# Optimization experiments

Measured on AMD Instinct MI355X. Metric: run time of the kernel, lower is better.

Reference implementation:

```python
import jax, jax.numpy as jnp
import numpy as np

D_MODEL = 256
SCALE = jnp.sqrt(jnp.float32(D_MODEL))


def setup_inputs() -> dict:
    key = jax.random.key(0)
    kq, kk, kv = jax.random.split(key, 3)
    B, S, D = 4, 4096, D_MODEL
    Q = jax.random.normal(kq, (B, S, D), dtype=jnp.float32)
    K = jax.random.normal(kk, (B, S, D), dtype=jnp.float32)
    V = jax.random.normal(kv, (B, S, D), dtype=jnp.float32)
    return {"Q": Q, "K": K, "V": V}


def reference(Q, K, V):
    # scores: (B, S, S) = Q @ K^T / sqrt(d_model)
    scores = jnp.einsum('bqd,bkd->bqk', Q, K) / SCALE
    attn = jax.nn.softmax(scores, axis=-1)
    # output: (B, S, D)
    return jnp.einsum('bqk,bkd->bqd', attn, V)
```

## Files before the change

### kernel.cpp

```cpp
#include <hip/hip_runtime.h>
#include <hip/hip_bf16.h>
#include <stdint.h>

#define S_LEN 4096
#define D_DIM 256
#define NBATCH 4
#define NSUP 32

typedef unsigned short u16;
typedef float  f32x4  __attribute__((ext_vector_type(4)));
typedef __bf16 bf16x8 __attribute__((ext_vector_type(8)));
typedef __bf16 bf16x4 __attribute__((ext_vector_type(4)));
typedef short  s16x8  __attribute__((ext_vector_type(8)));
typedef short  s16x4  __attribute__((ext_vector_type(4)));

#define AS1 __attribute__((address_space(1)))
#define AS3 __attribute__((address_space(3)))

__device__ __forceinline__ f32x4 mfma16(bf16x8 a, bf16x8 b, f32x4 c) {
  return __builtin_amdgcn_mfma_f32_16x16x32_bf16(a, b, c, 0, 0, 0);
}

__device__ __forceinline__ s16x4 cvt4(float x, float y, float z, float w) {
  bf16x4 b;
  b[0] = (__bf16)x; b[1] = (__bf16)y; b[2] = (__bf16)z; b[3] = (__bf16)w;
  return __builtin_bit_cast(s16x4, b);
}

__device__ __forceinline__ void gload16(const void* g, void* l) {
  __builtin_amdgcn_global_load_lds((const AS1 unsigned int*)g,
                                   (AS3 unsigned int*)l, 16, 0, 0);
}


__global__ void build_imgs(const float* __restrict__ K, const float* __restrict__ V,
                           u16* __restrict__ kimg, u16* __restrict__ vimg) {
  __shared__ u16 lds[64 * 264];
  const int wg  = blockIdx.x;
  const int tid = threadIdx.x;

  const float* ksrc = K + (size_t)wg * 64 * D_DIM;
  u16*         kdst = kimg + (size_t)wg * 16384;
  #pragma unroll
  for (int i = 0; i < 8; ++i) {
    const int idx = i * 256 + tid;
    const int k = idx >> 5, p = idx & 31;
    const int q = p ^ (k & 7);
    const float* s = ksrc + k * 256 + q * 8;
    float4 f0 = *reinterpret_cast<const float4*>(s);
    float4 f1 = *reinterpret_cast<const float4*>(s + 4);
    s16x8 v = __builtin_shufflevector(cvt4(f0.x, f0.y, f0.z, f0.w),
                                      cvt4(f1.x, f1.y, f1.z, f1.w),
                                      0, 1, 2, 3, 4, 5, 6, 7);
    *reinterpret_cast<s16x8*>(kdst + k * 256 + p * 8) = v;
  }

  const float* vsrc = V + (size_t)wg * 64 * D_DIM;
  u16*         vdst = vimg + (size_t)wg * 16384;
  #pragma unroll
  for (int i = 0; i < 8; ++i) {
    const int idx = i * 256 + tid;
    const int k = idx >> 5, q = idx & 31;
    const float* s = vsrc + k * 256 + q * 8;
    float4 f0 = *reinterpret_cast<const float4*>(s);
    float4 f1 = *reinterpret_cast<const float4*>(s + 4);
    s16x8 v = __builtin_shufflevector(cvt4(f0.x, f0.y, f0.z, f0.w),
                                      cvt4(f1.x, f1.y, f1.z, f1.w),
                                      0, 1, 2, 3, 4, 5, 6, 7);
    *reinterpret_cast<s16x8*>(&lds[k * 264 + q * 8]) = v;
  }
  __syncthreads();
  #pragma unroll
  for (int i = 0; i < 8; ++i) {
    const int idx = i * 256 + tid;
    const int d = idx >> 3, c = idx & 7;
    const int cp = c ^ (d & 7);
    s16x8 o;
    #pragma unroll
    for (int j = 0; j < 8; ++j) {
      const int col = 8 * cp + j;
      const int k = (col & 3) + 4 * (col >> 4) + 16 * ((col >> 2) & 3);
      o[j] = (short)lds[k * 264 + d];
    }
    *reinterpret_cast<s16x8*>(vdst + d * 64 + c * 8) = o;
  }
}

__device__ __forceinline__
void compute_tile(const char* KsB, const char* vpA, const char* vpB,
                  const bf16x8 (&qf)[8], f32x4 (&acc)[16],
                  float& m_run, float& l_run, int g, int h)
{
  const f32x4 fz = {0.f, 0.f, 0.f, 0.f};

  f32x4 st[4];
  __builtin_amdgcn_s_setprio(1);
  #pragma unroll
  for (int t = 0; t < 4; ++t) {
    f32x4 a = fz;
    const int row = t * 16 + h;
    const int sw  = (row & 7) << 4;
    #pragma unroll
    for (int dc = 0; dc < 8; ++dc) {
      s16x8 kfrag = *reinterpret_cast<const s16x8*>(KsB + row * 512 + ((dc * 64 + g * 16) ^ sw));
      a = mfma16(__builtin_bit_cast(bf16x8, kfrag), qf[dc], a);
    }
    st[t] = a;
  }
  __builtin_amdgcn_s_setprio(0);

  float sv[16];
  #pragma unroll
  for (int t = 0; t < 4; ++t) {
    sv[t * 4 + 0] = st[t][0]; sv[t * 4 + 1] = st[t][1];
    sv[t * 4 + 2] = st[t][2]; sv[t * 4 + 3] = st[t][3];
  }
  float tmax = sv[0];
  #pragma unroll
  for (int i = 1; i < 16; ++i) tmax = fmaxf(tmax, sv[i]);
  tmax = fmaxf(tmax, __shfl_xor(tmax, 16));
  tmax = fmaxf(tmax, __shfl_xor(tmax, 32));

  if (!__all(tmax <= m_run + 8.0f)) {
    const float mnew  = fmaxf(m_run, tmax);
    const float alpha = __expf(m_run - mnew);
    l_run *= alpha;
    const float af0 = __shfl(alpha, g * 4 + 0);
    const float af1 = __shfl(alpha, g * 4 + 1);
    const float af2 = __shfl(alpha, g * 4 + 2);
    const float af3 = __shfl(alpha, g * 4 + 3);
    #pragma unroll
    for (int dt = 0; dt < 16; ++dt) {
      acc[dt][0] *= af0; acc[dt][1] *= af1; acc[dt][2] *= af2; acc[dt][3] *= af3;
    }
    m_run = mnew;
  }

  float psum = 0.f;
  #pragma unroll
  for (int i = 0; i < 16; ++i) { sv[i] = __expf(sv[i] - m_run); psum += sv[i]; }
  psum += __shfl_xor(psum, 16);
  psum += __shfl_xor(psum, 32);
  l_run += psum;

  bf16x8 pa0, pa1;
  #pragma unroll
  for (int j = 0; j < 8; ++j) { pa0[j] = (__bf16)sv[j]; pa1[j] = (__bf16)sv[8 + j]; }

  __builtin_amdgcn_s_setprio(1);
  #pragma unroll
  for (int dt = 0; dt < 16; ++dt) {
    s16x8 v0 = *reinterpret_cast<const s16x8*>(vpA + dt * 2048);
    s16x8 v1 = *reinterpret_cast<const s16x8*>(vpB + dt * 2048);
    acc[dt] = mfma16(pa0, __builtin_bit_cast(bf16x8, v0), acc[dt]);
    acc[dt] = mfma16(pa1, __builtin_bit_cast(bf16x8, v1), acc[dt]);
  }
  __builtin_amdgcn_s_setprio(0);
}

__device__ __forceinline__
void stage_img(const u16* KimgB, const u16* VimgB, int T,
               char* KsB, char* VtB, int w, int lane)
{
  const char* ks = (const char*)(KimgB + (size_t)T * 16384) + lane * 16;
  const char* vs = (const char*)(VimgB + (size_t)T * 16384) + lane * 16;
  #pragma unroll
  for (int i = 0; i < 8; ++i) {
    const int off = (i * 4 + w) * 1024;
    gload16(ks + off, KsB + off);
    gload16(vs + off, VtB + off);
  }
}

template<bool USE_WS>
__global__ __launch_bounds__(512, 1)
void attn_fwd_kernel(const float* __restrict__ Qg, const void* __restrict__ Kp,
                     const void* __restrict__ Vp, float* __restrict__ Og)
{
  __shared__ __align__(16) char smem[131072];

  const int wg   = blockIdx.x;
  const int swz  = (wg & 7) * 32 + (wg >> 3);
  const int b    = swz >> 6;
  const int qt   = swz & 63;
  const int tid  = threadIdx.x;
  const int wave = tid >> 6;
  const int lane = tid & 63;
  const int g    = lane >> 4;
  const int h    = lane & 15;
  const int gid  = tid >> 8;
  const int ltid = tid & 255;
  const int wq   = wave & 3;
  const int w    = wave & 3;

  const int kb  = ltid & 15;
  const int dcq = ltid >> 4;
  const int Xw  = 32 * (kb & 3) + 8 * (kb >> 2);

  char* KsB = smem + gid * 65536;
  char* VtB = KsB + 32768;

  const int qbase = qt * 64 + wq * 16;

  bf16x8 qf[8];
  {
    const float* qrow = Qg + ((size_t)b * S_LEN + qbase + h) * D_DIM;
    #pragma unroll
    for (int dc = 0; dc < 8; ++dc) {
      float4 f0 = *reinterpret_cast<const float4*>(qrow + dc * 32 + g * 8);
      float4 f1 = *reinterpret_cast<const float4*>(qrow + dc * 32 + g * 8 + 4);
      bf16x8 q;
      q[0] = (__bf16)(f0.x * 0.0625f); q[1] = (__bf16)(f0.y * 0.0625f);
      q[2] = (__bf16)(f0.z * 0.0625f); q[3] = (__bf16)(f0.w * 0.0625f);
      q[4] = (__bf16)(f1.x * 0.0625f); q[5] = (__bf16)(f1.y * 0.0625f);
      q[6] = (__bf16)(f1.z * 0.0625f); q[7] = (__bf16)(f1.w * 0.0625f);
      qf[dc] = q;
    }
  }

  f32x4 acc[16];
  const f32x4 fz = {0.f, 0.f, 0.f, 0.f};
  #pragma unroll
  for (int i = 0; i < 16; ++i) acc[i] = fz;
  float m_run = -1e30f;
  float l_run = 0.f;

  const char* vpA = VtB + h * 128 + ((32 * g)      ^ ((h & 7) << 4));
  const char* vpB = VtB + h * 128 + ((32 * g + 16) ^ ((h & 7) << 4));

  if constexpr (USE_WS) {
    const u16* KimgB = (const u16*)Kp + (size_t)b * 64 * 16384;
    const u16* VimgB = (const u16*)Vp + (size_t)b * 64 * 16384;

    if (gid == 0) stage_img(KimgB, VimgB, 0, KsB, VtB, w, lane);
    __syncthreads();

    for (int s = 0; s < NSUP; ++s) {
      if (gid == 0) compute_tile(KsB, vpA, vpB, qf, acc, m_run, l_run, g, h);
      else          stage_img(KimgB, VimgB, 2 * s + 1, KsB, VtB, w, lane);
      __syncthreads();
      if (gid == 0) { if (s < NSUP - 1) stage_img(KimgB, VimgB, 2 * s + 2, KsB, VtB, w, lane); }
      else          compute_tile(KsB, vpA, vpB, qf, acc, m_run, l_run, g, h);
      __syncthreads();
    }

  } else {
    const float* Kf = (const float*)Kp + (size_t)b * S_LEN * D_DIM;
    const float* Vf = (const float*)Vp + (size_t)b * S_LEN * D_DIM;
    for (int s = 0; s < NSUP; ++s) {
      const int kt = 2 * s + gid;
      __syncthreads();
      #pragma unroll
      for (int i = 0; i < 16; ++i) {
        int flat = i * 256 + ltid;
        int kk = flat >> 6;
        int d  = (flat & 63) * 4;
        float4 fk = *reinterpret_cast<const float4*>(Kf + (size_t)(kt * 64 + kk) * D_DIM + d);
        *reinterpret_cast<s16x4*>(KsB + kk * 512 + ((d * 2) ^ ((kk & 7) << 4))) = cvt4(fk.x, fk.y, fk.z, fk.w);
      }
      {
        s16x8 lo[4], hi[4];
        #pragma unroll
        for (int r = 0; r < 4; ++r) {
          const float* src = Vf + (size_t)(kt * 64 + kb * 4 + r) * D_DIM + dcq * 16;
          float4 f0 = *reinterpret_cast<const float4*>(src);
          float4 f1 = *reinterpret_cast<const float4*>(src + 4);
          float4 f2 = *reinterpret_cast<const float4*>(src + 8);
          float4 f3 = *reinterpret_cast<const float4*>(src + 12);
          lo[r] = __builtin_shufflevector(cvt4(f0.x, f0.y, f0.z, f0.w),
                                          cvt4(f1.x, f1.y, f1.z, f1.w), 0, 1, 2, 3, 4, 5, 6, 7);
          hi[r] = __builtin_shufflevector(cvt4(f2.x, f2.y, f2.z, f2.w),
                                          cvt4(f3.x, f3.y, f3.z, f3.w), 0, 1, 2, 3, 4, 5, 6, 7);
        }
        #pragma unroll
        for (int j = 0; j < 8; ++j) {
          s16x4 c0, c1;
          c0[0] = lo[0][j]; c0[1] = lo[1][j]; c0[2] = lo[2][j]; c0[3] = lo[3][j];
          c1[0] = hi[0][j]; c1[1] = hi[1][j]; c1[2] = hi[2][j]; c1[3] = hi[3][j];
          const int d0 = dcq * 16 + j;
          const int d1 = d0 + 8;
          *reinterpret_cast<s16x4*>(VtB + d0 * 128 + (Xw ^ ((d0 & 7) << 4))) = c0;
          *reinterpret_cast<s16x4*>(VtB + d1 * 128 + (Xw ^ ((d1 & 7) << 4))) = c1;
        }
      }
      __syncthreads();
      compute_tile(KsB, vpA, vpB, qf, acc, m_run, l_run, g, h);
    }
  }

  __syncthreads();
  float2* mlM = reinterpret_cast<float2*>(smem + 65536);
  if (gid == 1) {
    const int bw = wave - 4;
    char* base = smem + bw * 16384 + lane * 256;
    #pragma unroll
    for (int dt = 0; dt < 16; ++dt) {
      float4 v; v.x = acc[dt][0]; v.y = acc[dt][1]; v.z = acc[dt][2]; v.w = acc[dt][3];
      *reinterpret_cast<float4*>(base + (dt * 16 ^ ((lane & 7) << 4))) = v;
    }
    if (g == 0) { float2 ml; ml.x = m_run; ml.y = l_run; mlM[bw * 16 + h] = ml; }
  }
  __syncthreads();
  if (gid == 0) {
    const float2 ml = mlM[wave * 16 + h];
    const float mB = ml.x, lB = ml.y;
    const float m  = fmaxf(m_run, mB);
    const float sA = __expf(m_run - m);
    const float sB = __expf(mB - m);
    const float l  = l_run * sA + lB * sB;
    float aA[4], aB[4], inv[4];
    #pragma unroll
    for (int r = 0; r < 4; ++r) {
      aA[r]  = __shfl(sA, g * 4 + r);
      aB[r]  = __shfl(sB, g * 4 + r);
      inv[r] = 1.f / __shfl(l, g * 4 + r);
    }
    const char* base = smem + wave * 16384 + lane * 256;
    float* orow0 = Og + ((size_t)b * S_LEN + qbase) * D_DIM;
    #pragma unroll
    for (int dt = 0; dt < 16; ++dt) {
      float4 ab = *reinterpret_cast<const float4*>(base + (dt * 16 ^ ((lane & 7) << 4)));
      orow0[(size_t)(g * 4 + 0) * D_DIM + h + dt * 16] = (acc[dt][0] * aA[0] + ab.x * aB[0]) * inv[0];
      orow0[(size_t)(g * 4 + 1) * D_DIM + h + dt * 16] = (acc[dt][1] * aA[1] + ab.y * aB[1]) * inv[1];
      orow0[(size_t)(g * 4 + 2) * D_DIM + h + dt * 16] = (acc[dt][2] * aA[2] + ab.z * aB[2]) * inv[2];
      orow0[(size_t)(g * 4 + 3) * D_DIM + h + dt * 16] = (acc[dt][3] * aA[3] + ab.w * aB[3]) * inv[3];
    }
  }
}

extern "C" void kernel_launch(void* const* d_in, const int* in_sizes, int n_in,
                              void* d_out, int out_size, void* d_ws, size_t ws_size,
                              hipStream_t stream)
{
  const float* Q = (const float*)d_in[0];
  const float* K = (const float*)d_in[1];
  const float* V = (const float*)d_in[2];
  float* O = (float*)d_out;

  const size_t nelem = (size_t)NBATCH * S_LEN * D_DIM;
  const size_t need  = 2 * nelem * sizeof(u16);

  if (ws_size >= need) {
    u16* Kimg = (u16*)d_ws;
    u16* Vimg = Kimg + nelem;
    build_imgs<<<256, 256, 0, stream>>>(K, V, Kimg, Vimg);
    attn_fwd_kernel<true><<<256, 512, 0, stream>>>(Q, (const void*)Kimg, (const void*)Vimg, O);
  } else {
    attn_fwd_kernel<false><<<256, 512, 0, stream>>>(Q, (const void*)K, (const void*)V, O);
  }
}
```

Baseline: 124.4 us.

## Split KV sequence in two halves with 32-row tiles and merge kernel

Adds a split-KV path. Each query tile is processed by two workgroups, one per half of the key sequence, using 32-row K/V tiles, smaller LDS and two workgroups per CU. Partial outputs and (m,l) statistics go to workspace and a separate merge kernel combines them. The aim is to double the grid from 256 to 512 workgroups for better CU occupancy, at the cost of extra global traffic for the fp32 partials, a third kernel launch, and half-width MFMA tiles per step.

```diff
diff --git a/kernel.cpp b/kernel.cpp
--- a/kernel.cpp
+++ b/kernel.cpp
@@ -5,7 +5,9 @@
 #define S_LEN 4096
 #define D_DIM 256
 #define NBATCH 4
-#define NSUP 32
+#define KVBLK 32
+#define NSUP32 32
+#define NSUP64 32
 
 typedef unsigned short u16;
 typedef float  f32x4  __attribute__((ext_vector_type(4)));
@@ -33,8 +35,60 @@
 }
 
 
-__global__ void build_imgs(const float* __restrict__ K, const float* __restrict__ V,
-                           u16* __restrict__ kimg, u16* __restrict__ vimg) {
+__global__ void build_imgs32(const float* __restrict__ K, const float* __restrict__ V,
+                             u16* __restrict__ kimg, u16* __restrict__ vimg) {
+  __shared__ u16 lds[KVBLK * 264];
+  const int wg  = blockIdx.x;
+  const int tid = threadIdx.x;
+
+  const float* ksrc = K + (size_t)wg * KVBLK * D_DIM;
+  u16*         kdst = kimg + (size_t)wg * 8192;
+  #pragma unroll
+  for (int i = 0; i < 4; ++i) {
+    const int idx = i * 256 + tid;
+    const int k = idx >> 5, p = idx & 31;
+    const int q = p ^ (k & 7);
+    const float* s = ksrc + k * 256 + q * 8;
+    float4 f0 = *reinterpret_cast<const float4*>(s);
+    float4 f1 = *reinterpret_cast<const float4*>(s + 4);
+    s16x8 v = __builtin_shufflevector(cvt4(f0.x, f0.y, f0.z, f0.w),
+                                      cvt4(f1.x, f1.y, f1.z, f1.w),
+                                      0, 1, 2, 3, 4, 5, 6, 7);
+    *reinterpret_cast<s16x8*>(kdst + k * 256 + p * 8) = v;
+  }
+
+  const float* vsrc = V + (size_t)wg * KVBLK * D_DIM;
+  u16*         vdst = vimg + (size_t)wg * 8192;
+  #pragma unroll
+  for (int i = 0; i < 4; ++i) {
+    const int idx = i * 256 + tid;
+    const int k = idx >> 5, q = idx & 31;
+    const float* s = vsrc + k * 256 + q * 8;
+    float4 f0 = *reinterpret_cast<const float4*>(s);
+    float4 f1 = *reinterpret_cast<const float4*>(s + 4);
+    s16x8 v = __builtin_shufflevector(cvt4(f0.x, f0.y, f0.z, f0.w),
+                                      cvt4(f1.x, f1.y, f1.z, f1.w),
+                                      0, 1, 2, 3, 4, 5, 6, 7);
+    *reinterpret_cast<s16x8*>(&lds[k * 264 + q * 8]) = v;
+  }
+  __syncthreads();
+  const int d = tid;
+  const int s = ((d >> 4) ^ d) & 3;
+  #pragma unroll
+  for (int c = 0; c < 4; ++c) {
+    const int gp = c ^ s;
+    s16x8 o;
+    #pragma unroll
+    for (int ii = 0; ii < 8; ++ii) {
+      const int k = 16 * (ii >> 2) + 4 * gp + (ii & 3);
+      o[ii] = (short)lds[k * 264 + d];
+    }
+    *reinterpret_cast<s16x8*>(vdst + d * 32 + c * 8) = o;
+  }
+}
+
+__global__ void build_imgs64(const float* __restrict__ K, const float* __restrict__ V,
+                             u16* __restrict__ kimg, u16* __restrict__ vimg) {
   __shared__ u16 lds[64 * 264];
   const int wg  = blockIdx.x;
   const int tid = threadIdx.x;
@@ -87,9 +141,79 @@
 }
 
 __device__ __forceinline__
-void compute_tile(const char* KsB, const char* vpA, const char* vpB,
-                  const bf16x8 (&qf)[8], f32x4 (&acc)[16],
-                  float& m_run, float& l_run, int g, int h)
+void compute_tile32(const char* KsB, const char* VtB,
+                    const bf16x8 (&qf)[8], f32x4 (&acc)[16],
+                    float& m_run, float& l_run, int g, int h)
+{
+  const f32x4 fz = {0.f, 0.f, 0.f, 0.f};
+
+  f32x4 st[2];
+  st[0] = fz; st[1] = fz;
+  __builtin_amdgcn_s_setprio(1);
+  #pragma unroll
+  for (int t = 0; t < 2; ++t) {
+    const int row = t * 16 + h;
+    const int sw  = (row & 7) << 4;
+    #pragma unroll
+    for (int dc = 0; dc < 8; ++dc) {
+      s16x8 kf = *reinterpret_cast<const s16x8*>(KsB + row * 512 + ((dc * 64 + g * 16) ^ sw));
+      st[t] = mfma16(__builtin_bit_cast(bf16x8, kf), qf[dc], st[t]);
+    }
+  }
+  __builtin_amdgcn_s_setprio(0);
+
+  float sv[8];
+  #pragma unroll
+  for (int t = 0; t < 2; ++t) {
+    sv[t * 4 + 0] = st[t][0]; sv[t * 4 + 1] = st[t][1];
+    sv[t * 4 + 2] = st[t][2]; sv[t * 4 + 3] = st[t][3];
+  }
+  float tmax = sv[0];
+  #pragma unroll
+  for (int i = 1; i < 8; ++i) tmax = fmaxf(tmax, sv[i]);
+  tmax = fmaxf(tmax, __shfl_xor(tmax, 16));
+  tmax = fmaxf(tmax, __shfl_xor(tmax, 32));
+
+  if (!__all(tmax <= m_run + 8.0f)) {
+    const float mnew  = fmaxf(m_run, tmax);
+    const float alpha = __expf(m_run - mnew);
+    l_run *= alpha;
+    float af[4];
+    #pragma unroll
+    for (int r = 0; r < 4; ++r) af[r] = __shfl(alpha, g * 4 + r);
+    #pragma unroll
+    for (int dt = 0; dt < 16; ++dt) {
+      acc[dt][0] *= af[0]; acc[dt][1] *= af[1];
+      acc[dt][2] *= af[2]; acc[dt][3] *= af[3];
+    }
+    m_run = mnew;
+  }
+
+  float psum = 0.f;
+  #pragma unroll
+  for (int i = 0; i < 8; ++i) { sv[i] = __expf(sv[i] - m_run); psum += sv[i]; }
+  psum += __shfl_xor(psum, 16);
+  psum += __shfl_xor(psum, 32);
+  l_run += psum;
+
+  bf16x8 pa;
+  #pragma unroll
+  for (int j = 0; j < 8; ++j) pa[j] = (__bf16)sv[j];
+
+  __builtin_amdgcn_s_setprio(1);
+  #pragma unroll
+  for (int dt = 0; dt < 16; ++dt) {
+    const int d = dt * 16 + h;
+    s16x8 vf = *reinterpret_cast<const s16x8*>(VtB + d * 64 + ((16 * g) ^ (((dt ^ h) & 3) << 4)));
+    acc[dt] = mfma16(pa, __builtin_bit_cast(bf16x8, vf), acc[dt]);
+  }
+  __builtin_amdgcn_s_setprio(0);
+}
+
+__device__ __forceinline__
+void compute_tile64(const char* KsB, const char* vpA, const char* vpB,
+                    const bf16x8 (&qf)[8], f32x4 (&acc)[16],
+                    float& m_run, float& l_run, int g, int h)
 {
   const f32x4 fz = {0.f, 0.f, 0.f, 0.f};
 
@@ -159,8 +283,21 @@
 }
 
 __device__ __forceinline__
-void stage_img(const u16* KimgB, const u16* VimgB, int T,
-               char* KsB, char* VtB, int w, int lane)
+void stage_img32(const u16* KimgB, const u16* VimgB, int T,
+                 char* KsB, char* VtB, int gl)
+{
+  const char* ks = (const char*)(KimgB + (size_t)T * 8192) + gl * 16;
+  const char* vs = (const char*)(VimgB + (size_t)T * 8192) + gl * 16;
+  #pragma unroll
+  for (int i = 0; i < 4; ++i) {
+    gload16(ks + i * 4096, KsB + gl * 16 + i * 4096);
+    gload16(vs + i * 4096, VtB + gl * 16 + i * 4096);
+  }
+}
+
+__device__ __forceinline__
+void stage_img64(const u16* KimgB, const u16* VimgB, int T,
+                 char* KsB, char* VtB, int w, int lane)
 {
   const char* ks = (const char*)(KimgB + (size_t)T * 16384) + lane * 16;
   const char* vs = (const char*)(VimgB + (size_t)T * 16384) + lane * 16;
@@ -172,9 +309,144 @@
   }
 }
 
+__global__ __launch_bounds__(512, 2)
+void attn_partial_kernel(const float* __restrict__ Qg, const u16* __restrict__ Kimg,
+                         const u16* __restrict__ Vimg, float* __restrict__ Opart,
+                         float2* __restrict__ mlG)
+{
+  __shared__ __align__(16) char smem[66560];
+
+  const int wg   = blockIdx.x;
+  const int swz  = (wg & 7) * 64 + (wg >> 3);
+  const int b    = swz >> 7;
+  const int half = (swz >> 6) & 1;
+  const int qt   = swz & 63;
+  const int tid  = threadIdx.x;
+  const int wave = tid >> 6;
+  const int lane = tid & 63;
+  const int g    = lane >> 4;
+  const int h    = lane & 15;
+  const int gid  = tid >> 8;
+  const int ltid = tid & 255;
+  const int wq   = wave & 3;
+
+  char* KsB = smem + gid * 32768;
+  char* VtB = KsB + 16384;
+  float2* mlM = reinterpret_cast<float2*>(smem + 65536);
+
+  const int qbase = qt * 64 + wq * 16;
+
+  bf16x8 qf[8];
+  {
+    const float* qrow = Qg + ((size_t)b * S_LEN + qbase + h) * D_DIM;
+    #pragma unroll
+    for (int dc = 0; dc < 8; ++dc) {
+      float4 f0 = *reinterpret_cast<const float4*>(qrow + dc * 32 + g * 8);
+      float4 f1 = *reinterpret_cast<const float4*>(qrow + dc * 32 + g * 8 + 4);
+      bf16x8 q;
+      q[0] = (__bf16)(f0.x * 0.0625f); q[1] = (__bf16)(f0.y * 0.0625f);
+      q[2] = (__bf16)(f0.z * 0.0625f); q[3] = (__bf16)(f0.w * 0.0625f);
+      q[4] = (__bf16)(f1.x * 0.0625f); q[5] = (__bf16)(f1.y * 0.0625f);
+      q[6] = (__bf16)(f1.z * 0.0625f); q[7] = (__bf16)(f1.w * 0.0625f);
+      qf[dc] = q;
+    }
+  }
+
+  f32x4 acc[16];
+  const f32x4 fz = {0.f, 0.f, 0.f, 0.f};
+  #pragma unroll
+  for (int i = 0; i < 16; ++i) acc[i] = fz;
+  float m_run = -1e30f;
+  float l_run = 0.f;
+
+  const u16* KimgB = Kimg + (size_t)b * 128 * 8192 + (size_t)half * 64 * 8192;
+  const u16* VimgB = Vimg + (size_t)b * 128 * 8192 + (size_t)half * 64 * 8192;
+
+  if (gid == 0) stage_img32(KimgB, VimgB, 0, KsB, VtB, ltid);
+  __syncthreads();
+  for (int s = 0; s < NSUP32; ++s) {
+    if (gid == 0) compute_tile32(KsB, VtB, qf, acc, m_run, l_run, g, h);
+    else          stage_img32(KimgB, VimgB, 2 * s + 1, KsB, VtB, ltid);
+    __syncthreads();
+    if (gid == 0) { if (s < NSUP32 - 1) stage_img32(KimgB, VimgB, 2 * s + 2, KsB, VtB, ltid); }
+    else          compute_tile32(KsB, VtB, qf, acc, m_run, l_run, g, h);
+    __syncthreads();
+  }
+
+  __syncthreads();
+  if (gid == 1) {
+    const int bw = wave - 4;
+    char* base = smem + bw * 16384 + lane * 256;
+    #pragma unroll
+    for (int dt = 0; dt < 16; ++dt) {
+      float4 v; v.x = acc[dt][0]; v.y = acc[dt][1]; v.z = acc[dt][2]; v.w = acc[dt][3];
+      *reinterpret_cast<float4*>(base + (dt * 16 ^ ((lane & 7) << 4))) = v;
+    }
+    if (g == 0) { float2 ml; ml.x = m_run; ml.y = l_run; mlM[bw * 16 + h] = ml; }
+  }
+  __syncthreads();
+  if (gid == 0) {
+    const float2 ml = mlM[wave * 16 + h];
+    const float mB = ml.x, lB = ml.y;
+    const float m  = fmaxf(m_run, mB);
+    const float sA = __expf(m_run - m);
+    const float sB = __expf(mB - m);
+    const float l  = l_run * sA + lB * sB;
+    float aA[4], aB[4];
+    #pragma unroll
+    for (int r = 0; r < 4; ++r) {
+      aA[r] = __shfl(sA, g * 4 + r);
+      aB[r] = __shfl(sB, g * 4 + r);
+    }
+    const char* base = smem + wave * 16384 + lane * 256;
+    float* orow0 = Opart + (size_t)half * NBATCH * S_LEN * D_DIM
+                 + ((size_t)b * S_LEN + qbase) * D_DIM;
+    #pragma unroll
+    for (int dt = 0; dt < 16; ++dt) {
+      float4 ab = *reinterpret_cast<const float4*>(base + (dt * 16 ^ ((lane & 7) << 4)));
+      orow0[(size_t)(g * 4 + 0) * D_DIM + h + dt * 16] = acc[dt][0] * aA[0] + ab.x * aB[0];
+      orow0[(size_t)(g * 4 + 1) * D_DIM + h + dt * 16] = acc[dt][1] * aA[1] + ab.y * aB[1];
+      orow0[(size_t)(g * 4 + 2) * D_DIM + h + dt * 16] = acc[dt][2] * aA[2] + ab.z * aB[2];
+      orow0[(size_t)(g * 4 + 3) * D_DIM + h + dt * 16] = acc[dt][3] * aA[3] + ab.w * aB[3];
+    }
+    if (g == 0) {
+      float2 o; o.x = m; o.y = l;
+      mlG[(size_t)half * NBATCH * S_LEN + (size_t)b * S_LEN + qbase + h] = o;
+    }
+  }
+}
+
+__global__ void merge_halves(const float* __restrict__ Opart,
+                             const float2* __restrict__ mlG,
+                             float* __restrict__ Og)
+{
+  const size_t TOT = (size_t)NBATCH * S_LEN * D_DIM;
+  const size_t f4base = ((size_t)blockIdx.x * 256 + threadIdx.x) * 4;
+  const size_t row = (f4base * 4) / D_DIM;
+  const float2 ml0 = mlG[row];
+  const float2 ml1 = mlG[(size_t)NBATCH * S_LEN + row];
+  const float m  = fmaxf(ml0.x, ml1.x);
+  const float w0 = __expf(ml0.x - m);
+  const float w1 = __expf(ml1.x - m);
+  const float inv = 1.f / (ml0.y * w0 + ml1.y * w1);
+  const float4* p0 = reinterpret_cast<const float4*>(Opart) + f4base;
+  const float4* p1 = reinterpret_cast<const float4*>(Opart + TOT) + f4base;
+  float4* po = reinterpret_cast<float4*>(Og) + f4base;
+  #pragma unroll
+  for (int i = 0; i < 4; ++i) {
+    float4 a = p0[i], c = p1[i];
+    float4 o;
+    o.x = (a.x * w0 + c.x * w1) * inv;
+    o.y = (a.y * w0 + c.y * w1) * inv;
+    o.z = (a.z * w0 + c.z * w1) * inv;
+    o.w = (a.w * w0 + c.w * w1) * inv;
+    po[i] = o;
+  }
+}
+
 template<bool USE_WS>
 __global__ __launch_bounds__(512, 1)
-void attn_fwd_kernel(const float* __restrict__ Qg, const void* __restrict__ Kp,
+void attn_r21_kernel(const float* __restrict__ Qg, const void* __restrict__ Kp,
                      const void* __restrict__ Vp, float* __restrict__ Og)
 {
   __shared__ __align__(16) char smem[131072];
@@ -232,22 +504,22 @@
     const u16* KimgB = (const u16*)Kp + (size_t)b * 64 * 16384;
     const u16* VimgB = (const u16*)Vp + (size_t)b * 64 * 16384;
 
-    if (gid == 0) stage_img(KimgB, VimgB, 0, KsB, VtB, w, lane);
+    if (gid == 0) stage_img64(KimgB, VimgB, 0, KsB, VtB, w, lane);
     __syncthreads();
 
-    for (int s = 0; s < NSUP; ++s) {
-      if (gid == 0) compute_tile(KsB, vpA, vpB, qf, acc, m_run, l_run, g, h);
-      else          stage_img(KimgB, VimgB, 2 * s + 1, KsB, VtB, w, lane);
+    for (int s = 0; s < NSUP64; ++s) {
+      if (gid == 0) compute_tile64(KsB, vpA, vpB, qf, acc, m_run, l_run, g, h);
+      else          stage_img64(KimgB, VimgB, 2 * s + 1, KsB, VtB, w, lane);
       __syncthreads();
-      if (gid == 0) { if (s < NSUP - 1) stage_img(KimgB, VimgB, 2 * s + 2, KsB, VtB, w, lane); }
-      else          compute_tile(KsB, vpA, vpB, qf, acc, m_run, l_run, g, h);
+      if (gid == 0) { if (s < NSUP64 - 1) stage_img64(KimgB, VimgB, 2 * s + 2, KsB, VtB, w, lane); }
+      else          compute_tile64(KsB, vpA, vpB, qf, acc, m_run, l_run, g, h);
       __syncthreads();
     }
 
   } else {
     const float* Kf = (const float*)Kp + (size_t)b * S_LEN * D_DIM;
     const float* Vf = (const float*)Vp + (size_t)b * S_LEN * D_DIM;
-    for (int s = 0; s < NSUP; ++s) {
+    for (int s = 0; s < NSUP64; ++s) {
       const int kt = 2 * s + gid;
       __syncthreads();
       #pragma unroll
@@ -284,7 +556,7 @@
         }
       }
       __syncthreads();
-      compute_tile(KsB, vpA, vpB, qf, acc, m_run, l_run, g, h);
+      compute_tile64(KsB, vpA, vpB, qf, acc, m_run, l_run, g, h);
     }
   }
 
@@ -337,15 +609,26 @@
   const float* V = (const float*)d_in[2];
   float* O = (float*)d_out;
 
-  const size_t nelem = (size_t)NBATCH * S_LEN * D_DIM;
-  const size_t need  = 2 * nelem * sizeof(u16);
-
-  if (ws_size >= need) {
+  const size_t nelem    = (size_t)NBATCH * S_LEN * D_DIM;
+  const size_t img_b    = 2 * nelem * sizeof(u16);
+  const size_t opart_b  = 2 * nelem * sizeof(float);
+  const size_t ml_b     = 2 * (size_t)NBATCH * S_LEN * sizeof(float2);
+  const size_t need_big = img_b + opart_b + ml_b;
+
+  if (ws_size >= need_big) {
+    u16*    Kimg  = (u16*)d_ws;
+    u16*    Vimg  = Kimg + nelem;
+    float*  Opart = (float*)((char*)d_ws + img_b);
+    float2* mlG   = (float2*)((char*)d_ws + img_b + opart_b);
+    build_imgs32<<<512, 256, 0, stream>>>(K, V, Kimg, Vimg);
+    attn_partial_kernel<<<512, 512, 0, stream>>>(Q, Kimg, Vimg, Opart, mlG);
+    merge_halves<<<1024, 256, 0, stream>>>(Opart, mlG, O);
+  } else if (ws_size >= img_b) {
     u16* Kimg = (u16*)d_ws;
     u16* Vimg = Kimg + nelem;
-    build_imgs<<<256, 256, 0, stream>>>(K, V, Kimg, Vimg);
-    attn_fwd_kernel<true><<<256, 512, 0, stream>>>(Q, (const void*)Kimg, (const void*)Vimg, O);
+    build_imgs64<<<256, 256, 0, stream>>>(K, V, Kimg, Vimg);
+    attn_r21_kernel<true><<<256, 512, 0, stream>>>(Q, (const void*)Kimg, (const void*)Vimg, O);
   } else {
-    attn_fwd_kernel<false><<<256, 512, 0, stream>>>(Q, (const void*)K, (const void*)V, O);
-  }
-}
+    attn_r21_kernel<false><<<256, 512, 0, stream>>>(Q, (const void*)K, (const void*)V, O);
+  }
+}
```

After: 176.2 us. +41.6%, slower.
